# Kernel optimization log

Measured on AMD Instinct MI355X. Metric: run time of the kernel, lower is better.

Reference implementation:

```python
import jax, jax.numpy as jnp
import numpy as np

LN_EPS = 1e-5
FACTOR = 4

def layer_norm(x, w, b):
    mu = jnp.mean(x, axis=-1, keepdims=True)
    var = jnp.mean((x - mu) ** 2, axis=-1, keepdims=True)
    return (x - mu) * jax.lax.rsqrt(var + LN_EPS) * w + b

def setup_inputs() -> dict:
    key = jax.random.key(0)
    k1, k2, k3 = jax.random.split(key, 3)
    B, Sq, Skv, D = 4, 2048, 8192, 1024
    return {
        "query": jax.random.normal(k1, (B, Sq, D), dtype=jnp.float32),
        "key": jax.random.normal(k2, (B, Skv, D), dtype=jnp.float32),
        "value": jax.random.normal(k3, (B, Skv, D), dtype=jnp.float32),
        "ln_weight": jnp.ones((D,), dtype=jnp.float32),
        "ln_bias": jnp.zeros((D,), dtype=jnp.float32),
    }

def attention_downsampling(q, k, v, factor):
    # q: [B, S//f, D], k/v: [B, S, D]
    B, S, D = k.shape
    k_win = k.reshape(B, S // factor, factor, D)
    weights = jnp.einsum('bsd,bsfd->bsf', q, k_win).reshape(B, S)  # no softmax
    attn = weights[:, :, None] * v                                  # [B, S, D]
    attn = attn.reshape(B, S // factor, factor, D).sum(axis=2)      # [B, S//f, D]
    return attn

def reference(query, key, value, ln_weight, ln_bias):
    # pre-norm (post_norm=False): residual + attention over normed q/k/v
    qn = layer_norm(query, ln_weight, ln_bias)
    kn = layer_norm(key, ln_weight, ln_bias)
    vn = layer_norm(value, ln_weight, ln_bias)
    return query + attention_downsampling(qn, kn, vn, FACTOR)
```

## Files before the change

kernel.cpp:

```cpp
#include <hip/hip_runtime.h>


typedef float f32x4 __attribute__((ext_vector_type(4)));

constexpr int D     = 1024;
constexpr int BLOCK = 256;
constexpr int NW    = BLOCK / 64;
constexpr int NRW   = 4;
constexpr float EPS = 1e-5f;

template<int CTRL>
__device__ __forceinline__ float dpp_add(float x) {
    int xi = __builtin_bit_cast(int, x);
    int yi = __builtin_amdgcn_update_dpp(0, xi, CTRL, 0xF, 0xF, true);
    return x + __builtin_bit_cast(float, yi);
}

__device__ __forceinline__ float wave_sum(float x) {
    x = dpp_add<0x111>(x);
    x = dpp_add<0x112>(x);
    x = dpp_add<0x114>(x);
    x = dpp_add<0x118>(x);
    x = dpp_add<0x142>(x);
    x = dpp_add<0x143>(x);
    return __builtin_bit_cast(float, __builtin_amdgcn_readlane(__builtin_bit_cast(int, x), 63));
}

__device__ __forceinline__ f32x4 vadd(f32x4 a, f32x4 b) {
    f32x4 r;
#pragma unroll
    for (int j = 0; j < 4; j++) r[j] = a[j] + b[j];
    return r;
}
__device__ __forceinline__ f32x4 vmul(f32x4 a, f32x4 b) {
    f32x4 r;
#pragma unroll
    for (int j = 0; j < 4; j++) r[j] = a[j] * b[j];
    return r;
}
__device__ __forceinline__ f32x4 vfma(f32x4 a, f32x4 b, f32x4 c) {
    f32x4 r;
#pragma unroll
    for (int j = 0; j < 4; j++) r[j] = fmaf(a[j], b[j], c[j]);
    return r;
}
__device__ __forceinline__ f32x4 vfma_ss(f32x4 a, float s, float c) {
    f32x4 r;
#pragma unroll
    for (int j = 0; j < 4; j++) r[j] = fmaf(a[j], s, c);
    return r;
}
__device__ __forceinline__ f32x4 vfma_sv(float s, f32x4 b, f32x4 c) {
    f32x4 r;
#pragma unroll
    for (int j = 0; j < 4; j++) r[j] = fmaf(s, b[j], c[j]);
    return r;
}
__device__ __forceinline__ float hsum(f32x4 a) { return (a[0] + a[1]) + (a[2] + a[3]); }

#define PIN4(A)  asm volatile("" :: "v"(A[0]), "v"(A[1]), "v"(A[2]), "v"(A[3]))
#define PIN16(A) asm volatile("" :: \
    "v"(A[0][0]), "v"(A[0][1]), "v"(A[0][2]), "v"(A[0][3]), \
    "v"(A[1][0]), "v"(A[1][1]), "v"(A[1][2]), "v"(A[1][3]), \
    "v"(A[2][0]), "v"(A[2][1]), "v"(A[2][2]), "v"(A[2][3]), \
    "v"(A[3][0]), "v"(A[3][1]), "v"(A[3][2]), "v"(A[3][3]))

__global__ __launch_bounds__(BLOCK, 2) void attn_ds_kernel(
    const float* __restrict__ q,
    const float* __restrict__ k,
    const float* __restrict__ v,
    const float* __restrict__ lw,
    const float* __restrict__ lb,
    float* __restrict__ out,
    int rows)
{
    const int  tid  = threadIdx.x;
    const int  lane = tid & 63;
    const int  wid  = tid >> 6;
    const int  sl   = lane * 4;
    const long gw   = (long)blockIdx.x * NW + wid;
    long r = gw * NRW;

    f32x4 wv[4], bv[4];
#pragma unroll
    for (int i = 0; i < 4; i++) {
        wv[i] = *(const f32x4*)(lw + i * 256 + sl);
        bv[i] = *(const f32x4*)(lb + i * 256 + sl);
    }
    f32x4 aw2 = {0.f, 0.f, 0.f, 0.f}, awb = {0.f, 0.f, 0.f, 0.f}, ab2 = {0.f, 0.f, 0.f, 0.f};
#pragma unroll
    for (int i = 0; i < 4; i++) {
        aw2 = vfma(wv[i], wv[i], aw2);
        awb = vfma(wv[i], bv[i], awb);
        ab2 = vfma(bv[i], bv[i], ab2);
    }
    const float Sw2 = wave_sum(hsum(aw2));
    const float Swb = wave_sum(hsum(awb));
    const float Sb2 = wave_sum(hsum(ab2));
    const float invD = 1.0f / (float)D;

#pragma unroll 1
    for (int rr = 0; rr < NRW; rr++, r++) {
        if (r >= rows) break;
        const float* qp = q + r * (long)D;
        const float* kp = k + r * (4L * D);
        const float* vp = v + r * (4L * D);

        f32x4 qv[4], kv[4][4], vv[4][4];
#pragma unroll
        for (int i = 0; i < 4; i++) qv[i] = *(const f32x4*)(qp + i * 256 + sl);
#pragma unroll
        for (int f = 0; f < 4; f++)
#pragma unroll
            for (int i = 0; i < 4; i++)
                kv[f][i] = *(const f32x4*)(kp + f * D + i * 256 + sl);
#pragma unroll
        for (int f = 0; f < 4; f++)
#pragma unroll
            for (int i = 0; i < 4; i++)
                vv[f][i] = *(const f32x4*)(vp + f * D + i * 256 + sl);

        PIN16(kv);
        PIN16(vv);
        PIN4(qv);
        __builtin_amdgcn_sched_barrier(0);

        f32x4 qw[4];
#pragma unroll
        for (int i = 0; i < 4; i++) qw[i] = vmul(qv[i], wv[i]);

        float pSk[4], pSkk[4], pSkw2[4], pSkwb[4], pA[4];
#pragma unroll
        for (int f = 0; f < 4; f++) {
            f32x4 s = {0.f,0.f,0.f,0.f}, ss = s, sw2a = s, swba = s, sA = s;
#pragma unroll
            for (int i = 0; i < 4; i++) {
                f32x4 kk = kv[f][i];
                s    = vadd(s, kk);
                ss   = vfma(kk, kk, ss);
                f32x4 t = vmul(kk, wv[i]);
                sw2a = vfma(t, wv[i], sw2a);
                swba = vfma(t, bv[i], swba);
                sA   = vfma(t, qw[i], sA);
            }
            pSk[f] = hsum(s); pSkk[f] = hsum(ss);
            pSkw2[f] = hsum(sw2a); pSkwb[f] = hsum(swba); pA[f] = hsum(sA);
        }

        f32x4 a0 = {0.f,0.f,0.f,0.f}, a1 = a0, a2 = a0, a3 = a0;
#pragma unroll
        for (int i = 0; i < 4; i++) {
            a0 = vadd(a0, qv[i]);
            a1 = vfma(qv[i], qv[i], a1);
            a2 = vfma(qw[i], wv[i], a2);
            a3 = vfma(qw[i], bv[i], a3);
        }
        float pSq = hsum(a0), pSqq = hsum(a1), pSqw2 = hsum(a2), pSqwb = hsum(a3);

        float pSv[4], pSvv[4];
#pragma unroll
        for (int f = 0; f < 4; f++) {
            f32x4 s = {0.f,0.f,0.f,0.f}, ss = s;
#pragma unroll
            for (int i = 0; i < 4; i++) {
                s  = vadd(s, vv[f][i]);
                ss = vfma(vv[f][i], vv[f][i], ss);
            }
            pSv[f] = hsum(s); pSvv[f] = hsum(ss);
        }

        const float Sq   = wave_sum(pSq);
        const float Sqq  = wave_sum(pSqq);
        const float Sqw2 = wave_sum(pSqw2);
        const float Sqwb = wave_sum(pSqwb);
        float Sk[4], Skk[4], Skw2[4], Skwb[4], A[4], Sv[4], Svv[4];
#pragma unroll
        for (int f = 0; f < 4; f++) {
            Sk[f]   = wave_sum(pSk[f]);
            Skk[f]  = wave_sum(pSkk[f]);
            Skw2[f] = wave_sum(pSkw2[f]);
            Skwb[f] = wave_sum(pSkwb[f]);
            A[f]    = wave_sum(pA[f]);
            Sv[f]   = wave_sum(pSv[f]);
            Svv[f]  = wave_sum(pSvv[f]);
        }

        const float mu_q = Sq * invD;
        const float rs_q = rsqrtf(fmaf(-mu_q, mu_q, Sqq * invD) + EPS);
        const float qlin = rs_q * (Sqwb - mu_q * Swb);
        float dp[4], rs_v[4], cv[4];
#pragma unroll
        for (int f = 0; f < 4; f++) {
            const float mu_k = Sk[f] * invD;
            const float rs_k = rsqrtf(fmaf(-mu_k, mu_k, Skk[f] * invD) + EPS);
            const float mu_v = Sv[f] * invD;
            const float rv   = rsqrtf(fmaf(-mu_v, mu_v, Svv[f] * invD) + EPS);
            const float cross = A[f] - mu_k * Sqw2 - mu_q * Skw2[f] + mu_q * mu_k * Sw2;
            dp[f] = rs_q * rs_k * cross + qlin + rs_k * (Skwb[f] - mu_k * Swb) + Sb2;
            rs_v[f] = rv;
            cv[f]   = -mu_v * rv;
        }

#pragma unroll
        for (int i = 0; i < 4; i++) {
            f32x4 acc = qv[i];
#pragma unroll
            for (int f = 0; f < 4; f++) {
                f32x4 t  = vfma_ss(vv[f][i], rs_v[f], cv[f]);
                f32x4 vn = vfma(t, wv[i], bv[i]);
                acc = vfma_sv(dp[f], vn, acc);
            }
            *(f32x4*)(out + r * (long)D + i * 256 + sl) = acc;
        }
    }
}

extern "C" void kernel_launch(void* const* d_in, const int* in_sizes, int n_in,
                              void* d_out, int out_size, void* d_ws, size_t ws_size,
                              hipStream_t stream) {
    const float* q  = (const float*)d_in[0];
    const float* k  = (const float*)d_in[1];
    const float* v  = (const float*)d_in[2];
    const float* lw = (const float*)d_in[3];
    const float* lb = (const float*)d_in[4];
    float* out = (float*)d_out;

    const int rows = in_sizes[0] / D;
    const int grid = (rows + NW * NRW - 1) / (NW * NRW);
    attn_ds_kernel<<<dim3(grid), dim3(BLOCK), 0, stream>>>(q, k, v, lw, lb, out, rows);
}
```

Before: 317.7 us.

## Stage V rows into LDS via direct global-to-LDS loads and double-buffer K

V tiles now go straight from global memory into per-wave LDS using global_load_lds, instead of being held in 64 VGPRs. K is streamed through two register buffers so loads overlap the per-row reductions, and each wave handles one output row instead of four, so the grid is four times larger. The aim is lower register pressure and more memory parallelism for this bandwidth-bound kernel. In exchange it adds 64KB of LDS per block, which may cap occupancy, and w/b setup is recomputed once per row.

```diff
diff --git a/kernel.cpp b/kernel.cpp
--- a/kernel.cpp
+++ b/kernel.cpp
@@ -6,8 +6,10 @@
 constexpr int D     = 1024;
 constexpr int BLOCK = 256;
 constexpr int NW    = BLOCK / 64;
-constexpr int NRW   = 4;
 constexpr float EPS = 1e-5f;
+
+#define GLOBAL_AS const __attribute__((address_space(1))) void*
+#define LDS_AS __attribute__((address_space(3))) void*
 
 template<int CTRL>
 __device__ __forceinline__ float dpp_add(float x) {
@@ -58,12 +60,7 @@
 }
 __device__ __forceinline__ float hsum(f32x4 a) { return (a[0] + a[1]) + (a[2] + a[3]); }
 
-#define PIN4(A)  asm volatile("" :: "v"(A[0]), "v"(A[1]), "v"(A[2]), "v"(A[3]))
-#define PIN16(A) asm volatile("" :: \
-    "v"(A[0][0]), "v"(A[0][1]), "v"(A[0][2]), "v"(A[0][3]), \
-    "v"(A[1][0]), "v"(A[1][1]), "v"(A[1][2]), "v"(A[1][3]), \
-    "v"(A[2][0]), "v"(A[2][1]), "v"(A[2][2]), "v"(A[2][3]), \
-    "v"(A[3][0]), "v"(A[3][1]), "v"(A[3][2]), "v"(A[3][3]))
+#define PINW(A) asm volatile("" :: "v"(A[0]), "v"(A[1]), "v"(A[2]), "v"(A[3]))
 
 __global__ __launch_bounds__(BLOCK, 2) void attn_ds_kernel(
     const float* __restrict__ q,
@@ -74,97 +71,109 @@
     float* __restrict__ out,
     int rows)
 {
+    __shared__ float v_lds[NW][4 * D];
+
     const int  tid  = threadIdx.x;
     const int  lane = tid & 63;
     const int  wid  = tid >> 6;
     const int  sl   = lane * 4;
-    const long gw   = (long)blockIdx.x * NW + wid;
-    long r = gw * NRW;
-
-    f32x4 wv[4], bv[4];
-#pragma unroll
-    for (int i = 0; i < 4; i++) {
-        wv[i] = *(const f32x4*)(lw + i * 256 + sl);
-        bv[i] = *(const f32x4*)(lb + i * 256 + sl);
-    }
-    f32x4 aw2 = {0.f, 0.f, 0.f, 0.f}, awb = {0.f, 0.f, 0.f, 0.f}, ab2 = {0.f, 0.f, 0.f, 0.f};
-#pragma unroll
-    for (int i = 0; i < 4; i++) {
-        aw2 = vfma(wv[i], wv[i], aw2);
-        awb = vfma(wv[i], bv[i], awb);
-        ab2 = vfma(bv[i], bv[i], ab2);
-    }
-    const float Sw2 = wave_sum(hsum(aw2));
-    const float Swb = wave_sum(hsum(awb));
-    const float Sb2 = wave_sum(hsum(ab2));
-    const float invD = 1.0f / (float)D;
-
-#pragma unroll 1
-    for (int rr = 0; rr < NRW; rr++, r++) {
-        if (r >= rows) break;
+    const long r    = (long)blockIdx.x * NW + wid;
+
+    if (r < rows) {
         const float* qp = q + r * (long)D;
         const float* kp = k + r * (4L * D);
         const float* vp = v + r * (4L * D);
-
-        f32x4 qv[4], kv[4][4], vv[4][4];
+        float* vl = &v_lds[wid][0];
+
+#pragma unroll
+        for (int c = 0; c < 16; c++)
+            __builtin_amdgcn_global_load_lds((GLOBAL_AS)(vp + c * 256 + sl),
+                                             (LDS_AS)(vl + c * 256), 16, 0, 0);
+
+        f32x4 wv[4], bv[4];
+#pragma unroll
+        for (int i = 0; i < 4; i++) {
+            wv[i] = *(const f32x4*)(lw + i * 256 + sl);
+            bv[i] = *(const f32x4*)(lb + i * 256 + sl);
+        }
+        f32x4 aw2 = {0.f,0.f,0.f,0.f}, awb = aw2, ab2 = aw2;
+#pragma unroll
+        for (int i = 0; i < 4; i++) {
+            aw2 = vfma(wv[i], wv[i], aw2);
+            awb = vfma(wv[i], bv[i], awb);
+            ab2 = vfma(bv[i], bv[i], ab2);
+        }
+        const float Sw2 = wave_sum(hsum(aw2));
+        const float Swb = wave_sum(hsum(awb));
+        const float Sb2 = wave_sum(hsum(ab2));
+        const float invD = 1.0f / (float)D;
+
+        f32x4 qv[4], qw[4];
 #pragma unroll
         for (int i = 0; i < 4; i++) qv[i] = *(const f32x4*)(qp + i * 256 + sl);
-#pragma unroll
-        for (int f = 0; f < 4; f++)
-#pragma unroll
-            for (int i = 0; i < 4; i++)
-                kv[f][i] = *(const f32x4*)(kp + f * D + i * 256 + sl);
-#pragma unroll
-        for (int f = 0; f < 4; f++)
-#pragma unroll
-            for (int i = 0; i < 4; i++)
-                vv[f][i] = *(const f32x4*)(vp + f * D + i * 256 + sl);
-
-        PIN16(kv);
-        PIN16(vv);
-        PIN4(qv);
-        __builtin_amdgcn_sched_barrier(0);
-
-        f32x4 qw[4];
-#pragma unroll
-        for (int i = 0; i < 4; i++) qw[i] = vmul(qv[i], wv[i]);
-
-        float pSk[4], pSkk[4], pSkw2[4], pSkwb[4], pA[4];
-#pragma unroll
-        for (int f = 0; f < 4; f++) {
-            f32x4 s = {0.f,0.f,0.f,0.f}, ss = s, sw2a = s, swba = s, sA = s;
-#pragma unroll
-            for (int i = 0; i < 4; i++) {
-                f32x4 kk = kv[f][i];
-                s    = vadd(s, kk);
-                ss   = vfma(kk, kk, ss);
-                f32x4 t = vmul(kk, wv[i]);
-                sw2a = vfma(t, wv[i], sw2a);
-                swba = vfma(t, bv[i], swba);
-                sA   = vfma(t, qw[i], sA);
-            }
-            pSk[f] = hsum(s); pSkk[f] = hsum(ss);
-            pSkw2[f] = hsum(sw2a); pSkwb[f] = hsum(swba); pA[f] = hsum(sA);
-        }
-
+        PINW(qv);
         f32x4 a0 = {0.f,0.f,0.f,0.f}, a1 = a0, a2 = a0, a3 = a0;
 #pragma unroll
         for (int i = 0; i < 4; i++) {
+            qw[i] = vmul(qv[i], wv[i]);
             a0 = vadd(a0, qv[i]);
             a1 = vfma(qv[i], qv[i], a1);
             a2 = vfma(qw[i], wv[i], a2);
             a3 = vfma(qw[i], bv[i], a3);
         }
-        float pSq = hsum(a0), pSqq = hsum(a1), pSqw2 = hsum(a2), pSqwb = hsum(a3);
-
+        const float pSq = hsum(a0), pSqq = hsum(a1), pSqw2 = hsum(a2), pSqwb = hsum(a3);
+
+        float pSk[4], pSkk[4], pSkw2[4], pSkwb[4], pA[4];
+        f32x4 kw0[4], kw1[4];
+#pragma unroll
+        for (int i = 0; i < 4; i++) kw0[i] = *(const f32x4*)(kp + 0 * D + i * 256 + sl);
+#pragma unroll
+        for (int i = 0; i < 4; i++) kw1[i] = *(const f32x4*)(kp + 1 * D + i * 256 + sl);
+        PINW(kw0); PINW(kw1);
+        __builtin_amdgcn_sched_barrier(0);
+
+#define PROCK(f, KK) { \
+        f32x4 s = {0.f,0.f,0.f,0.f}, ss = s, sw2a = s, swba = s, sA = s; \
+        _Pragma("unroll") \
+        for (int i = 0; i < 4; i++) { \
+            f32x4 kk = KK[i]; \
+            s    = vadd(s, kk); \
+            ss   = vfma(kk, kk, ss); \
+            f32x4 t = vmul(kk, wv[i]); \
+            sw2a = vfma(t, wv[i], sw2a); \
+            swba = vfma(t, bv[i], swba); \
+            sA   = vfma(t, qw[i], sA); \
+        } \
+        pSk[f] = hsum(s); pSkk[f] = hsum(ss); \
+        pSkw2[f] = hsum(sw2a); pSkwb[f] = hsum(swba); pA[f] = hsum(sA); }
+
+        PROCK(0, kw0);
+#pragma unroll
+        for (int i = 0; i < 4; i++) kw0[i] = *(const f32x4*)(kp + 2 * D + i * 256 + sl);
+        PINW(kw0);
+        __builtin_amdgcn_sched_barrier(0);
+
+        PROCK(1, kw1);
+#pragma unroll
+        for (int i = 0; i < 4; i++) kw1[i] = *(const f32x4*)(kp + 3 * D + i * 256 + sl);
+        PINW(kw1);
+        __builtin_amdgcn_sched_barrier(0);
+
+        PROCK(2, kw0);
+        PROCK(3, kw1);
+#undef PROCK
+
+        asm volatile("s_waitcnt vmcnt(0) lgkmcnt(0)" ::: "memory");
+        __builtin_amdgcn_sched_barrier(0);
         float pSv[4], pSvv[4];
 #pragma unroll
         for (int f = 0; f < 4; f++) {
             f32x4 s = {0.f,0.f,0.f,0.f}, ss = s;
 #pragma unroll
             for (int i = 0; i < 4; i++) {
-                s  = vadd(s, vv[f][i]);
-                ss = vfma(vv[f][i], vv[f][i], ss);
+                f32x4 vvif = *(const f32x4*)(vl + f * D + i * 256 + sl);
+                s  = vadd(s, vvif);
+                ss = vfma(vvif, vvif, ss);
             }
             pSv[f] = hsum(s); pSvv[f] = hsum(ss);
         }
@@ -206,7 +215,8 @@
             f32x4 acc = qv[i];
 #pragma unroll
             for (int f = 0; f < 4; f++) {
-                f32x4 t  = vfma_ss(vv[f][i], rs_v[f], cv[f]);
+                f32x4 vvif = *(const f32x4*)(vl + f * D + i * 256 + sl);
+                f32x4 t  = vfma_ss(vvif, rs_v[f], cv[f]);
                 f32x4 vn = vfma(t, wv[i], bv[i]);
                 acc = vfma_sv(dp[f], vn, acc);
             }
@@ -226,6 +236,6 @@
     float* out = (float*)d_out;
 
     const int rows = in_sizes[0] / D;
-    const int grid = (rows + NW * NRW - 1) / (NW * NRW);
+    const int grid = (rows + NW - 1) / NW;
     attn_ds_kernel<<<dim3(grid), dim3(BLOCK), 0, stream>>>(q, k, v, lw, lb, out, rows);
 }
```

After: 311.6 us. No clear change (-1.9%).
